# Performance work log

Hardware: AMD Instinct MI355X
Metric: run time of the kernel (lower is better)

## Reference

```python
import math
import jax, jax.numpy as jnp
import numpy as np

NUM_HEAD = 16
BLOCK_SIZE = 2048

def get_slopes(n):
    def pow2(n):
        start = 2 ** (-2 ** (-(math.log2(n) - 3)))
        return [start * start ** i for i in range(n)]
    if math.log2(n).is_integer():
        return pow2(n)
    c = 2 ** math.floor(math.log2(n))
    return pow2(c) + get_slopes(2 * c)[0::2][: n - c]

def setup_inputs() -> dict:
    key = jax.random.key(0)
    ks = jax.random.split(key, 5)
    B, T, C = 4, 2048, 1024
    x = jax.random.normal(ks[0], (B, T, C), dtype=jnp.float32)
    Wq = 0.02 * jax.random.normal(ks[1], (C, C), dtype=jnp.float32)
    Wk = 0.02 * jax.random.normal(ks[2], (C, C), dtype=jnp.float32)
    Wv = 0.02 * jax.random.normal(ks[3], (C, C), dtype=jnp.float32)
    Wo = 0.02 * jax.random.normal(ks[4], (C, C), dtype=jnp.float32)
    return {"x": x, "Wq": Wq, "Wk": Wk, "Wv": Wv, "Wo": Wo}

def reference(x, Wq, Wk, Wv, Wo):
    B, T, C = x.shape
    nh, hd = NUM_HEAD, C // NUM_HEAD
    # projections, split heads -> [B, nh, T, hd]
    q = (x @ Wq).reshape(B, T, nh, hd).transpose(0, 2, 1, 3)
    k = (x @ Wk).reshape(B, T, nh, hd).transpose(0, 2, 1, 3)
    v = (x @ Wv).reshape(B, T, nh, hd).transpose(0, 2, 1, 3)
    # full [B, nh, T, T] scores (module materializes these)
    attn = jnp.einsum("bhqd,bhkd->bhqk", q, k) / jnp.sqrt(jnp.float32(hd))
    # ALiBi bias as in create_mask: slope * (j - (block_size - 1)), key-position only
    slopes = jnp.asarray(get_slopes(nh), dtype=jnp.float32)  # [nh]
    bias = slopes[:, None] * (jnp.arange(T, dtype=jnp.float32) - (BLOCK_SIZE - 1))  # [nh, T]
    attn = attn + bias[None, :, None, :]
    # causal mask + stable softmax in fp32
    causal = jnp.tril(jnp.ones((T, T), dtype=bool))
    masked = jnp.where(causal[None, None], attn.astype(jnp.float32), jnp.finfo(jnp.float32).min)
    probs = jax.nn.softmax(masked, axis=-1)
    out = jnp.einsum("bhqk,bhkd->bhqd", probs, v)  # [B, nh, T, hd]
    out = out.transpose(0, 2, 1, 3).reshape(B, T, C)
    return out @ Wo
```

## Files before the change

kernel.cpp:

```cpp
#include <hip/hip_runtime.h>
#include <hip/hip_bf16.h>

#define TSEQ   2048
#define CDIM   1024
#define NHEAD  16
#define HDIM   64

typedef float f32x4  __attribute__((ext_vector_type(4)));
typedef float f32x16v __attribute__((ext_vector_type(16)));
typedef __bf16 bf16x8 __attribute__((ext_vector_type(8)));
typedef unsigned short u16x8 __attribute__((ext_vector_type(8)));
typedef unsigned short u16x4 __attribute__((ext_vector_type(4)));
typedef unsigned int   u32x4 __attribute__((ext_vector_type(4)));

#define QSCALE 0.18033688011112042f
#define LOG2E  1.4426950408889634f

static __device__ __forceinline__ unsigned short f2bf(float f) {
    unsigned u = __builtin_bit_cast(unsigned, f);
    unsigned r = u + 0x7FFFu + ((u >> 16) & 1u);
    return (unsigned short)(r >> 16);
}

static __device__ __forceinline__ f32x4 mfma16(u16x8 a, u16x8 b, f32x4 c) {
    return __builtin_amdgcn_mfma_f32_16x16x32_bf16(
        __builtin_bit_cast(bf16x8, a), __builtin_bit_cast(bf16x8, b), c, 0, 0, 0);
}
static __device__ __forceinline__ f32x16v mfma32(u16x8 a, u16x8 b, f32x16v c) {
    return __builtin_amdgcn_mfma_f32_32x32x16_bf16(
        __builtin_bit_cast(bf16x8, a), __builtin_bit_cast(bf16x8, b), c, 0, 0, 0);
}

static __device__ __forceinline__ void gload16(const void* g, void* l) {
    __builtin_amdgcn_global_load_lds(
        (const __attribute__((address_space(1))) unsigned int*)g,
        (__attribute__((address_space(3))) unsigned int*)l, 16, 0, 0);
}


__global__ __launch_bounds__(256) void castx(
    const float* __restrict__ x, unsigned short* __restrict__ xb)
{
    int t = blockIdx.x * 256 + threadIdx.x;
    f32x4 v = *(const f32x4*)&x[t * 4];
    u16x4 o;
    o[0] = f2bf(v[0]); o[1] = f2bf(v[1]); o[2] = f2bf(v[2]); o[3] = f2bf(v[3]);
    *(u16x4*)&xb[t * 4] = o;
}

__global__ __launch_bounds__(256) void wtcast(
    const float* __restrict__ wq, const float* __restrict__ wk,
    const float* __restrict__ wv, const float* __restrict__ wo,
    unsigned short* __restrict__ wt)
{
    __shared__ unsigned short t[64 * 72];
    const int z = blockIdx.z;
    const float* src = (z == 0) ? wq : (z == 1) ? wk : (z == 2) ? wv : wo;
    const int k0 = blockIdx.x * 64, n0 = blockIdx.y * 64, tid = threadIdx.x;

    #pragma unroll
    for (int i = 0; i < 4; ++i) {
        int idx = i * 256 + tid;
        int r = idx >> 4, c4 = idx & 15;
        f32x4 v = *(const f32x4*)&src[(k0 + r) * 1024 + n0 + c4 * 4];
        u16x4 o;
        o[0] = f2bf(v[0]); o[1] = f2bf(v[1]); o[2] = f2bf(v[2]); o[3] = f2bf(v[3]);
        *(u16x4*)&t[r * 72 + c4 * 4] = o;
    }
    __syncthreads();
    #pragma unroll
    for (int i = 0; i < 2; ++i) {
        int idx = i * 256 + tid;
        int n = idx >> 3, k8 = idx & 7;
        u16x8 o;
        #pragma unroll
        for (int e = 0; e < 8; ++e) o[e] = t[(k8 * 8 + e) * 72 + n];
        *(u16x8*)&wt[z * 1048576 + (n0 + n) * 1024 + k0 + k8 * 8] = o;
    }
}

template<int MODE>
__global__ __launch_bounds__(256) void gemm_gl(
    const unsigned short* __restrict__ A, const unsigned short* __restrict__ WT,
    unsigned short* __restrict__ outb, float* __restrict__ outf)
{
    __shared__ __align__(16) unsigned short Al[128 * 64];
    __shared__ __align__(16) unsigned short Bl[128 * 64];

    const int tid  = threadIdx.x;
    const int z    = blockIdx.z;
    const int m0   = blockIdx.y * 128;
    const int n0   = blockIdx.x * 128;
    const unsigned short* W = WT + (MODE == 0 ? z * 1048576 : 0);

    const int wid  = tid >> 6, lane = tid & 63;
    const int wr   = (wid >> 1) * 64, wc = (wid & 1) * 64;
    const int lrow = lane & 15, lk = (lane >> 4) * 8;

    f32x4 acc[4][4] = {};

    for (int kt = 0; kt < 16; ++kt) {
        __syncthreads();
        #pragma unroll
        for (int c = 0; c < 4; ++c) {
            int cz = wid * 4 + c;
            int row = cz * 8 + (lane >> 3), col = (lane & 7) * 8;
            gload16(&A[(m0 + row) * 1024 + kt * 64 + col], &Al[cz * 512]);
            gload16(&W[(n0 + row) * 1024 + kt * 64 + col], &Bl[cz * 512]);
        }
        __syncthreads();
        #pragma unroll
        for (int ks = 0; ks < 2; ++ks) {
            u16x8 af[4], bfr[4];
            #pragma unroll
            for (int m = 0; m < 4; ++m)
                af[m] = *(const u16x8*)&Al[(wr + m * 16 + lrow) * 64 + ks * 32 + lk];
            #pragma unroll
            for (int n = 0; n < 4; ++n)
                bfr[n] = *(const u16x8*)&Bl[(wc + n * 16 + lrow) * 64 + ks * 32 + lk];
            #pragma unroll
            for (int m = 0; m < 4; ++m)
                #pragma unroll
                for (int n = 0; n < 4; ++n)
                    acc[m][n] = mfma16(af[m], bfr[n], acc[m][n]);
        }
    }

    const int g = lane >> 4;
    #pragma unroll
    for (int m = 0; m < 4; ++m)
        #pragma unroll
        for (int n = 0; n < 4; ++n)
            #pragma unroll
            for (int j = 0; j < 4; ++j) {
                int grow = m0 + wr + m * 16 + g * 4 + j;
                int gcol = n0 + wc + n * 16 + lrow;
                float val = acc[m][n][j];
                if (MODE == 0) {
                    int b = grow >> 11, t = grow & 2047;
                    int h = gcol >> 6,  d = gcol & 63;
                    if (z == 0) val *= QSCALE;
                    if (z == 2)
                        outb[z * 8388608 + (((b << 4) + h) * 64 + d) * 2048 + t] = f2bf(val);
                    else
                        outb[z * 8388608 + (((b << 4) + h) * 2048 + t) * 64 + d] = f2bf(val);
                } else {
                    outf[grow * 1024 + gcol] = val;
                }
            }
}

__global__ __launch_bounds__(256) void attn128(
    const unsigned short* __restrict__ qh, const unsigned short* __restrict__ kh,
    const unsigned short* __restrict__ vt, unsigned short* __restrict__ aout)
{
    __shared__ __align__(16) unsigned short Kl[2][128 * 64];
    __shared__ __align__(16) unsigned short Vl[2][64 * 128];

    const int j   = blockIdx.x;
    const int bh  = blockIdx.y;
    const int h   = bh & 15, b = bh >> 4;
    const int tid = threadIdx.x, wid = tid >> 6, lane = tid & 63;
    const int l31 = lane & 31, hi = lane >> 5;

    const int blkA = 15 - j, blkB = j;
    const int ntA  = blkA + 1;
    const int nt   = 17;

    const unsigned short* Qb = qh + bh * (TSEQ * HDIM);
    const unsigned short* Kb = kh + bh * (TSEQ * HDIM);
    const unsigned short* Vb = vt + bh * (TSEQ * HDIM);

    const float slope2 = exp2f(-0.5f * (float)(h + 1)) * LOG2E;

    const int krow = lane >> 3;
    const int kgc  = (lane & 7) ^ krow;
    const int vrow = lane >> 4;
    const int vcc  = lane & 15;

#define STAGE(BUF, KV) do {                                                   \
    _Pragma("unroll")                                                         \
    for (int i_ = 0; i_ < 4; ++i_) {                                          \
        int g_ = wid * 4 + i_;                                                \
        gload16(&Kb[((KV) + g_ * 8 + krow) * 64 + kgc * 8],                   \
                &Kl[BUF][g_ * 512]);                                          \
        int d_ = g_ * 4 + vrow;                                               \
        int gc_ = vcc ^ (d_ & 15);                                            \
        gload16(&Vb[d_ * 2048 + (KV) + gc_ * 8], &Vl[BUF][g_ * 512]);         \
    } } while (0)

    int qw = blkA * 128 + wid * 32;
    int qg = qw + l31;
    u16x8 qf[4];
    #pragma unroll
    for (int kf = 0; kf < 4; ++kf)
        qf[kf] = *(const u16x8*)&Qb[qg * 64 + kf * 16 + hi * 8];
    float m_r = -1e30f, l_r = 0.f;
    f32x16v Ot[2] = {};

    STAGE(0, 0);
    int cur = 0;

    for (int t = 0; t < nt; ++t) {
        const int kv0 = (t < ntA ? t : t - ntA) * 128;
        __syncthreads();

        if (t + 1 < nt) {
            const int t1 = t + 1;
            const int kv0n = (t1 < ntA ? t1 : t1 - ntA) * 128;
            STAGE(cur ^ 1, kv0n);
        }

        f32x16v st[4];
        __builtin_amdgcn_s_setprio(1);
        #pragma unroll
        for (int kv2 = 0; kv2 < 4; ++kv2) {
            f32x16v a = {};
            #pragma unroll
            for (int kf = 0; kf < 4; ++kf) {
                u16x8 ka = *(const u16x8*)&Kl[cur][(kv2 * 32 + l31) * 64 +
                                                   (((kf * 2 + hi) ^ (l31 & 7)) * 8)];
                a = mfma32(ka, qf[kf], a);
            }
            st[kv2] = a;
        }
        __builtin_amdgcn_s_setprio(0);

        const bool diag = (kv0 + 127 > qw);
        #pragma unroll
        for (int kv2 = 0; kv2 < 4; ++kv2) {
            float base = slope2 * (float)(kv0 + kv2 * 32 + 4 * hi - 2047);
            #pragma unroll
            for (int r = 0; r < 16; ++r) {
                int koff = (r & 3) + 8 * (r >> 2);
                float v = st[kv2][r] + fmaf(slope2, (float)koff, base);
                if (diag) {
                    int kv = kv0 + kv2 * 32 + koff + 4 * hi;
                    if (kv > qg) v = -1e30f;
                }
                st[kv2][r] = v;
            }
        }

        float t16[16];
        #pragma unroll
        for (int i = 0; i < 16; ++i)
            t16[i] = fmaxf(fmaxf(st[0][i], st[1][i]), fmaxf(st[2][i], st[3][i]));
        #pragma unroll
        for (int i = 0; i < 8; ++i) t16[i] = fmaxf(t16[i], t16[i + 8]);
        #pragma unroll
        for (int i = 0; i < 4; ++i) t16[i] = fmaxf(t16[i], t16[i + 4]);
        float rm = fmaxf(fmaxf(t16[0], t16[1]), fmaxf(t16[2], t16[3]));
        rm = fmaxf(rm, __shfl_xor(rm, 32, 64));

        if (!__all(rm - m_r <= 8.0f)) {
            float mn = fmaxf(m_r, rm);
            float alpha = exp2f(m_r - mn);
            m_r = mn;
            l_r *= alpha;
            Ot[0] *= alpha;
            Ot[1] *= alpha;
        }

        #pragma unroll
        for (int kv2 = 0; kv2 < 4; ++kv2)
            #pragma unroll
            for (int r = 0; r < 16; ++r)
                st[kv2][r] = exp2f(st[kv2][r] - m_r);
        float s16[16];
        #pragma unroll
        for (int i = 0; i < 16; ++i)
            s16[i] = (st[0][i] + st[1][i]) + (st[2][i] + st[3][i]);
        #pragma unroll
        for (int i = 0; i < 8; ++i) s16[i] += s16[i + 8];
        #pragma unroll
        for (int i = 0; i < 4; ++i) s16[i] += s16[i + 4];
        float rs = (s16[0] + s16[1]) + (s16[2] + s16[3]);
        rs += __shfl_xor(rs, 32, 64);
        l_r += rs;

        unsigned pku[4][8];
        #pragma unroll
        for (int kv2 = 0; kv2 < 4; ++kv2)
            #pragma unroll
            for (int idx = 0; idx < 8; ++idx) {
                unsigned lo = __builtin_bit_cast(unsigned short, (__bf16)st[kv2][2 * idx]);
                unsigned hh = __builtin_bit_cast(unsigned short, (__bf16)st[kv2][2 * idx + 1]);
                pku[kv2][idx] = lo | (hh << 16);
            }

        u16x8 pb[8];
        #pragma unroll
        for (int kf = 0; kf < 8; ++kf) {
            const int kv2 = kf >> 1, base = 4 * (kf & 1);
            unsigned s0 = hi ? pku[kv2][base + 0] : pku[kv2][base + 2];
            unsigned s1 = hi ? pku[kv2][base + 1] : pku[kv2][base + 3];
            unsigned r0 = __shfl_xor(s0, 32, 64);
            unsigned r1 = __shfl_xor(s1, 32, 64);
            u32x4 w;
            w[0] = hi ? r0 : pku[kv2][base + 0];
            w[1] = hi ? r1 : pku[kv2][base + 1];
            w[2] = hi ? pku[kv2][base + 2] : r0;
            w[3] = hi ? pku[kv2][base + 3] : r1;
            pb[kf] = __builtin_bit_cast(u16x8, w);
        }

        __builtin_amdgcn_s_setprio(1);
        #pragma unroll
        for (int dn = 0; dn < 2; ++dn) {
            f32x16v o = Ot[dn];
            #pragma unroll
            for (int kf = 0; kf < 8; ++kf) {
                u16x8 va = *(const u16x8*)&Vl[cur][(dn * 32 + l31) * 128 +
                                                   (((kf * 2 + hi) ^ (l31 & 15)) * 8)];
                o = mfma32(va, pb[kf], o);
            }
            Ot[dn] = o;
        }
        __builtin_amdgcn_s_setprio(0);

        if (t == ntA - 1) {
            float rl = 1.0f / l_r;
            #pragma unroll
            for (int dn = 0; dn < 2; ++dn)
                #pragma unroll
                for (int rq = 0; rq < 4; ++rq) {
                    u16x4 o;
                    #pragma unroll
                    for (int jj = 0; jj < 4; ++jj)
                        o[jj] = f2bf(Ot[dn][rq * 4 + jj] * rl);
                    int d = dn * 32 + 8 * rq + 4 * hi;
                    *(u16x4*)&aout[(b * 2048 + qg) * 1024 + h * 64 + d] = o;
                }
            qw = blkB * 128 + wid * 32;
            qg = qw + l31;
            #pragma unroll
            for (int kf = 0; kf < 4; ++kf)
                qf[kf] = *(const u16x8*)&Qb[qg * 64 + kf * 16 + hi * 8];
            m_r = -1e30f; l_r = 0.f;
            Ot[0] = (f32x16v){};
            Ot[1] = (f32x16v){};
        }

        cur ^= 1;
    }

    float rl = 1.0f / l_r;
    #pragma unroll
    for (int dn = 0; dn < 2; ++dn)
        #pragma unroll
        for (int rq = 0; rq < 4; ++rq) {
            u16x4 o;
            #pragma unroll
            for (int jj = 0; jj < 4; ++jj)
                o[jj] = f2bf(Ot[dn][rq * 4 + jj] * rl);
            int d = dn * 32 + 8 * rq + 4 * hi;
            *(u16x4*)&aout[(b * 2048 + qg) * 1024 + h * 64 + d] = o;
        }
#undef STAGE
}

extern "C" void kernel_launch(void* const* d_in, const int* in_sizes, int n_in,
                              void* d_out, int out_size, void* d_ws, size_t ws_size,
                              hipStream_t stream)
{
    const float* x  = (const float*)d_in[0];
    const float* Wq = (const float*)d_in[1];
    const float* Wk = (const float*)d_in[2];
    const float* Wv = (const float*)d_in[3];
    const float* Wo = (const float*)d_in[4];

    unsigned short* ws = (unsigned short*)d_ws;
    unsigned short* wb = ws;
    unsigned short* xb = ws + 4194304;
    unsigned short* qh = ws + 12582912;
    unsigned short* kh = qh + 8388608;
    unsigned short* vt = kh + 8388608;
    unsigned short* ao = xb;

    castx<<<dim3(8192), dim3(256), 0, stream>>>(x, xb);
    wtcast<<<dim3(16, 16, 4), dim3(256), 0, stream>>>(Wq, Wk, Wv, Wo, wb);
    gemm_gl<0><<<dim3(8, 64, 3), dim3(256), 0, stream>>>(xb, wb, qh, (float*)nullptr);
    attn128<<<dim3(8, 64), dim3(256), 0, stream>>>(qh, kh, vt, ao);
    gemm_gl<1><<<dim3(8, 64, 1), dim3(256), 0, stream>>>(
        ao, wb + 3 * 1048576, (unsigned short*)nullptr, (float*)d_out);
}
```

Measured before the change: 238.6 us.

## Use 256-row query tiles with 512-thread blocks and skip masked sub-tiles

The attention kernel no longer pairs two 128-row query blocks per workgroup for load balance. Each 512-thread workgroup now handles one 256-row query block, iterating over its causal KV range, and blocks are launched heaviest-first. Diagonal tiles compute only the 32-key sub-blocks that are not fully masked, which cuts MFMA, exp and PV work. The cost is uneven per-block work, since the paired balancing is gone, and heavier register and LDS demand per workgroup under launch_bounds(512,4).

Measured after the change: 436.2 us. 1.83x slower.

```diff
diff --git a/kernel.cpp b/kernel.cpp
--- a/kernel.cpp
+++ b/kernel.cpp
@@ -150,22 +150,22 @@
             }
 }
 
-__global__ __launch_bounds__(256) void attn128(
+__global__ __launch_bounds__(512, 4) void attn256(
     const unsigned short* __restrict__ qh, const unsigned short* __restrict__ kh,
     const unsigned short* __restrict__ vt, unsigned short* __restrict__ aout)
 {
     __shared__ __align__(16) unsigned short Kl[2][128 * 64];
     __shared__ __align__(16) unsigned short Vl[2][64 * 128];
 
-    const int j   = blockIdx.x;
+    const int c   = 7 - blockIdx.x;
     const int bh  = blockIdx.y;
     const int h   = bh & 15, b = bh >> 4;
     const int tid = threadIdx.x, wid = tid >> 6, lane = tid & 63;
     const int l31 = lane & 31, hi = lane >> 5;
 
-    const int blkA = 15 - j, blkB = j;
-    const int ntA  = blkA + 1;
-    const int nt   = 17;
+    const int ntiles = 2 * c + 2;
+    const int qw = c * 256 + wid * 32;
+    const int qg = qw + l31;
 
     const unsigned short* Qb = qh + bh * (TSEQ * HDIM);
     const unsigned short* Kb = kh + bh * (TSEQ * HDIM);
@@ -180,166 +180,156 @@
 
 #define STAGE(BUF, KV) do {                                                   \
     _Pragma("unroll")                                                         \
-    for (int i_ = 0; i_ < 4; ++i_) {                                          \
-        int g_ = wid * 4 + i_;                                                \
-        gload16(&Kb[((KV) + g_ * 8 + krow) * 64 + kgc * 8],                   \
-                &Kl[BUF][g_ * 512]);                                          \
-        int d_ = g_ * 4 + vrow;                                               \
+    for (int i_ = 0; i_ < 2; ++i_) {                                          \
+        int cz_ = wid * 2 + i_;                                    \
+        gload16(&Kb[((KV) + cz_ * 8 + krow) * 64 + kgc * 8],                  \
+                &Kl[BUF][cz_ * 512]);                                         \
+        int d_ = cz_ * 4 + vrow;                                              \
         int gc_ = vcc ^ (d_ & 15);                                            \
-        gload16(&Vb[d_ * 2048 + (KV) + gc_ * 8], &Vl[BUF][g_ * 512]);         \
+        gload16(&Vb[d_ * 2048 + (KV) + gc_ * 8], &Vl[BUF][cz_ * 512]);        \
     } } while (0)
 
-    int qw = blkA * 128 + wid * 32;
-    int qg = qw + l31;
     u16x8 qf[4];
     #pragma unroll
     for (int kf = 0; kf < 4; ++kf)
         qf[kf] = *(const u16x8*)&Qb[qg * 64 + kf * 16 + hi * 8];
+
     float m_r = -1e30f, l_r = 0.f;
     f32x16v Ot[2] = {};
 
     STAGE(0, 0);
     int cur = 0;
 
-    for (int t = 0; t < nt; ++t) {
-        const int kv0 = (t < ntA ? t : t - ntA) * 128;
+    for (int t = 0; t < ntiles; ++t) {
+        const int kv0 = t * 128;
         __syncthreads();
 
-        if (t + 1 < nt) {
-            const int t1 = t + 1;
-            const int kv0n = (t1 < ntA ? t1 : t1 - ntA) * 128;
-            STAGE(cur ^ 1, kv0n);
-        }
-
-        f32x16v st[4];
-        __builtin_amdgcn_s_setprio(1);
-        #pragma unroll
-        for (int kv2 = 0; kv2 < 4; ++kv2) {
-            f32x16v a = {};
-            #pragma unroll
-            for (int kf = 0; kf < 4; ++kf) {
-                u16x8 ka = *(const u16x8*)&Kl[cur][(kv2 * 32 + l31) * 64 +
-                                                   (((kf * 2 + hi) ^ (l31 & 7)) * 8)];
-                a = mfma32(ka, qf[kf], a);
-            }
-            st[kv2] = a;
-        }
-        __builtin_amdgcn_s_setprio(0);
+        if (t + 1 < ntiles) STAGE(cur ^ 1, (t + 1) * 128);
 
         const bool diag = (kv0 + 127 > qw);
-        #pragma unroll
-        for (int kv2 = 0; kv2 < 4; ++kv2) {
-            float base = slope2 * (float)(kv0 + kv2 * 32 + 4 * hi - 2047);
-            #pragma unroll
-            for (int r = 0; r < 16; ++r) {
-                int koff = (r & 3) + 8 * (r >> 2);
-                float v = st[kv2][r] + fmaf(slope2, (float)koff, base);
-                if (diag) {
-                    int kv = kv0 + kv2 * 32 + koff + 4 * hi;
-                    if (kv > qg) v = -1e30f;
-                }
-                st[kv2][r] = v;
-            }
-        }
-
-        float t16[16];
-        #pragma unroll
-        for (int i = 0; i < 16; ++i)
-            t16[i] = fmaxf(fmaxf(st[0][i], st[1][i]), fmaxf(st[2][i], st[3][i]));
-        #pragma unroll
-        for (int i = 0; i < 8; ++i) t16[i] = fmaxf(t16[i], t16[i + 8]);
-        #pragma unroll
-        for (int i = 0; i < 4; ++i) t16[i] = fmaxf(t16[i], t16[i + 4]);
-        float rm = fmaxf(fmaxf(t16[0], t16[1]), fmaxf(t16[2], t16[3]));
-        rm = fmaxf(rm, __shfl_xor(rm, 32, 64));
-
-        if (!__all(rm - m_r <= 8.0f)) {
-            float mn = fmaxf(m_r, rm);
-            float alpha = exp2f(m_r - mn);
-            m_r = mn;
-            l_r *= alpha;
-            Ot[0] *= alpha;
-            Ot[1] *= alpha;
-        }
-
-        #pragma unroll
-        for (int kv2 = 0; kv2 < 4; ++kv2)
-            #pragma unroll
-            for (int r = 0; r < 16; ++r)
-                st[kv2][r] = exp2f(st[kv2][r] - m_r);
-        float s16[16];
-        #pragma unroll
-        for (int i = 0; i < 16; ++i)
-            s16[i] = (st[0][i] + st[1][i]) + (st[2][i] + st[3][i]);
-        #pragma unroll
-        for (int i = 0; i < 8; ++i) s16[i] += s16[i + 8];
-        #pragma unroll
-        for (int i = 0; i < 4; ++i) s16[i] += s16[i + 4];
-        float rs = (s16[0] + s16[1]) + (s16[2] + s16[3]);
-        rs += __shfl_xor(rs, 32, 64);
-        l_r += rs;
-
-        unsigned pku[4][8];
-        #pragma unroll
-        for (int kv2 = 0; kv2 < 4; ++kv2)
-            #pragma unroll
-            for (int idx = 0; idx < 8; ++idx) {
-                unsigned lo = __builtin_bit_cast(unsigned short, (__bf16)st[kv2][2 * idx]);
-                unsigned hh = __builtin_bit_cast(unsigned short, (__bf16)st[kv2][2 * idx + 1]);
-                pku[kv2][idx] = lo | (hh << 16);
-            }
-
-        u16x8 pb[8];
-        #pragma unroll
-        for (int kf = 0; kf < 8; ++kf) {
-            const int kv2 = kf >> 1, base = 4 * (kf & 1);
-            unsigned s0 = hi ? pku[kv2][base + 0] : pku[kv2][base + 2];
-            unsigned s1 = hi ? pku[kv2][base + 1] : pku[kv2][base + 3];
-            unsigned r0 = __shfl_xor(s0, 32, 64);
-            unsigned r1 = __shfl_xor(s1, 32, 64);
-            u32x4 w;
-            w[0] = hi ? r0 : pku[kv2][base + 0];
-            w[1] = hi ? r1 : pku[kv2][base + 1];
-            w[2] = hi ? pku[kv2][base + 2] : r0;
-            w[3] = hi ? pku[kv2][base + 3] : r1;
-            pb[kf] = __builtin_bit_cast(u16x8, w);
-        }
-
-        __builtin_amdgcn_s_setprio(1);
-        #pragma unroll
-        for (int dn = 0; dn < 2; ++dn) {
-            f32x16v o = Ot[dn];
+        int nkv2 = 4;
+        if (diag) {
+            int v = qw - kv0;
+            nkv2 = (v < 0) ? 0 : ((v >> 5) + 1);
+            if (nkv2 > 4) nkv2 = 4;
+        }
+
+        if (nkv2 > 0) {
+            f32x16v st[4];
+            __builtin_amdgcn_s_setprio(1);
+            #pragma unroll
+            for (int kv2 = 0; kv2 < 4; ++kv2) {
+                if (kv2 < nkv2) {
+                    f32x16v a = {};
+                    #pragma unroll
+                    for (int kf = 0; kf < 4; ++kf) {
+                        u16x8 ka = *(const u16x8*)&Kl[cur][(kv2 * 32 + l31) * 64 +
+                                                           (((kf * 2 + hi) ^ (l31 & 7)) * 8)];
+                        a = mfma32(ka, qf[kf], a);
+                    }
+                    st[kv2] = a;
+                } else {
+                    st[kv2] = (f32x16v)(-1e30f);
+                }
+            }
+            __builtin_amdgcn_s_setprio(0);
+
+            #pragma unroll
+            for (int kv2 = 0; kv2 < 4; ++kv2) {
+                if (kv2 < nkv2) {
+                    float base = slope2 * (float)(kv0 + kv2 * 32 + 4 * hi - 2047);
+                    #pragma unroll
+                    for (int r = 0; r < 16; ++r) {
+                        int koff = (r & 3) + 8 * (r >> 2);
+                        float v = st[kv2][r] + fmaf(slope2, (float)koff, base);
+                        if (diag) {
+                            int kv = kv0 + kv2 * 32 + koff + 4 * hi;
+                            if (kv > qg) v = -1e30f;
+                        }
+                        st[kv2][r] = v;
+                    }
+                }
+            }
+
+            float t16[16];
+            #pragma unroll
+            for (int i = 0; i < 16; ++i)
+                t16[i] = fmaxf(fmaxf(st[0][i], st[1][i]), fmaxf(st[2][i], st[3][i]));
+            #pragma unroll
+            for (int i = 0; i < 8; ++i) t16[i] = fmaxf(t16[i], t16[i + 8]);
+            #pragma unroll
+            for (int i = 0; i < 4; ++i) t16[i] = fmaxf(t16[i], t16[i + 4]);
+            float rm = fmaxf(fmaxf(t16[0], t16[1]), fmaxf(t16[2], t16[3]));
+            rm = fmaxf(rm, __shfl_xor(rm, 32, 64));
+
+            if (!__all(rm - m_r <= 8.0f)) {
+                float mn = fmaxf(m_r, rm);
+                float alpha = exp2f(m_r - mn);
+                m_r = mn;
+                l_r *= alpha;
+                Ot[0] *= alpha;
+                Ot[1] *= alpha;
+            }
+
+            #pragma unroll
+            for (int kv2 = 0; kv2 < 4; ++kv2) {
+                if (kv2 < nkv2) {
+                    #pragma unroll
+                    for (int r = 0; r < 16; ++r)
+                        st[kv2][r] = exp2f(st[kv2][r] - m_r);
+                } else {
+                    st[kv2] = (f32x16v)(0.f);
+                }
+            }
+            float s16[16];
+            #pragma unroll
+            for (int i = 0; i < 16; ++i)
+                s16[i] = (st[0][i] + st[1][i]) + (st[2][i] + st[3][i]);
+            #pragma unroll
+            for (int i = 0; i < 8; ++i) s16[i] += s16[i + 8];
+            #pragma unroll
+            for (int i = 0; i < 4; ++i) s16[i] += s16[i + 4];
+            float rs = (s16[0] + s16[1]) + (s16[2] + s16[3]);
+            rs += __shfl_xor(rs, 32, 64);
+            l_r += rs;
+
+            unsigned pku[4][8];
+            #pragma unroll
+            for (int kv2 = 0; kv2 < 4; ++kv2) {
+                if (kv2 < nkv2) {
+                    #pragma unroll
+                    for (int idx = 0; idx < 8; ++idx) {
+                        unsigned lo = __builtin_bit_cast(unsigned short, (__bf16)st[kv2][2 * idx]);
+                        unsigned hh = __builtin_bit_cast(unsigned short, (__bf16)st[kv2][2 * idx + 1]);
+                        pku[kv2][idx] = lo | (hh << 16);
+                    }
+                }
+            }
+
+            __builtin_amdgcn_s_setprio(1);
             #pragma unroll
             for (int kf = 0; kf < 8; ++kf) {
-                u16x8 va = *(const u16x8*)&Vl[cur][(dn * 32 + l31) * 128 +
-                                                   (((kf * 2 + hi) ^ (l31 & 15)) * 8)];
-                o = mfma32(va, pb[kf], o);
-            }
-            Ot[dn] = o;
-        }
-        __builtin_amdgcn_s_setprio(0);
-
-        if (t == ntA - 1) {
-            float rl = 1.0f / l_r;
-            #pragma unroll
-            for (int dn = 0; dn < 2; ++dn)
-                #pragma unroll
-                for (int rq = 0; rq < 4; ++rq) {
-                    u16x4 o;
-                    #pragma unroll
-                    for (int jj = 0; jj < 4; ++jj)
-                        o[jj] = f2bf(Ot[dn][rq * 4 + jj] * rl);
-                    int d = dn * 32 + 8 * rq + 4 * hi;
-                    *(u16x4*)&aout[(b * 2048 + qg) * 1024 + h * 64 + d] = o;
-                }
-            qw = blkB * 128 + wid * 32;
-            qg = qw + l31;
-            #pragma unroll
-            for (int kf = 0; kf < 4; ++kf)
-                qf[kf] = *(const u16x8*)&Qb[qg * 64 + kf * 16 + hi * 8];
-            m_r = -1e30f; l_r = 0.f;
-            Ot[0] = (f32x16v){};
-            Ot[1] = (f32x16v){};
+                if ((kf >> 1) < nkv2) {
+                    const int kv2 = kf >> 1, base = 4 * (kf & 1);
+                    unsigned s0 = hi ? pku[kv2][base + 0] : pku[kv2][base + 2];
+                    unsigned s1 = hi ? pku[kv2][base + 1] : pku[kv2][base + 3];
+                    unsigned r0 = __shfl_xor(s0, 32, 64);
+                    unsigned r1 = __shfl_xor(s1, 32, 64);
+                    u32x4 w;
+                    w[0] = hi ? r0 : pku[kv2][base + 0];
+                    w[1] = hi ? r1 : pku[kv2][base + 1];
+                    w[2] = hi ? pku[kv2][base + 2] : r0;
+                    w[3] = hi ? pku[kv2][base + 3] : r1;
+                    u16x8 pb = __builtin_bit_cast(u16x8, w);
+                    #pragma unroll
+                    for (int dn = 0; dn < 2; ++dn) {
+                        u16x8 va = *(const u16x8*)&Vl[cur][(dn * 32 + l31) * 128 +
+                                                           (((kf * 2 + hi) ^ (l31 & 15)) * 8)];
+                        Ot[dn] = mfma32(va, pb, Ot[dn]);
+                    }
+                }
+            }
+            __builtin_amdgcn_s_setprio(0);
         }
 
         cur ^= 1;
@@ -381,7 +371,7 @@
     castx<<<dim3(8192), dim3(256), 0, stream>>>(x, xb);
     wtcast<<<dim3(16, 16, 4), dim3(256), 0, stream>>>(Wq, Wk, Wv, Wo, wb);
     gemm_gl<0><<<dim3(8, 64, 3), dim3(256), 0, stream>>>(xb, wb, qh, (float*)nullptr);
-    attn128<<<dim3(8, 64), dim3(256), 0, stream>>>(qh, kh, vt, ao);
+    attn256<<<dim3(8, 64), dim3(512), 0, stream>>>(qh, kh, vt, ao);
     gemm_gl<1><<<dim3(8, 64, 1), dim3(256), 0, stream>>>(
         ao, wb + 3 * 1048576, (unsigned short*)nullptr, (float*)d_out);
 }
```
